# Kernel optimization log

Hardware: AMD Instinct MI355X
Metric: run time of the kernel (lower is better)

The kernel has to match this reference:

```python
import jax, jax.numpy as jnp
import numpy as np

B, N, C_IN, C_OUT, K = 16, 4096, 3, 64, 20
EPS = 1e-5


def setup_inputs() -> dict:
    key = jax.random.key(0)
    ks = jax.random.split(key, 6)
    x = jax.random.normal(ks[0], (B * N, C_IN), dtype=jnp.float32)
    batch = jnp.repeat(jnp.arange(B, dtype=jnp.int32), N)
    # MLP([2*C_IN, C_OUT, C_OUT]) per PyG: Linear -> BatchNorm -> ReLU -> Linear (plain last)
    w1 = jax.random.normal(ks[1], (2 * C_IN, C_OUT), dtype=jnp.float32) / np.sqrt(2 * C_IN)
    b1 = jnp.zeros((C_OUT,), dtype=jnp.float32)
    gamma = jnp.ones((C_OUT,), dtype=jnp.float32)
    beta = jnp.zeros((C_OUT,), dtype=jnp.float32)
    w2 = jax.random.normal(ks[2], (C_OUT, C_OUT), dtype=jnp.float32) / np.sqrt(C_OUT)
    b2 = jnp.zeros((C_OUT,), dtype=jnp.float32)
    return {"x": x, "batch": batch, "w1": w1, "b1": b1,
            "gamma": gamma, "beta": beta, "w2": w2, "b2": b2}


def reference(x, batch, w1, b1, gamma, beta, w2, b2):
    # batch is sorted with equal-size clouds -> reshape to [B, N, C]
    xb = x.reshape(B, N, C_IN)
    # pairwise squared distances within each cloud: [B, N, N]
    sq = jnp.sum(xb * xb, axis=-1)
    d = sq[:, :, None] + sq[:, None, :] - 2.0 * jnp.einsum('bnc,bmc->bnm', xb, xb)
    # k nearest neighbors (self included, matching PyG knn): [B, N, K]
    idx = jax.lax.top_k(-d, K)[1]
    # gather neighbor features: [B, N, K, C]
    xj = jax.vmap(lambda pts, ind: pts[ind])(xb, idx)
    xi = xb[:, :, None, :]
    # edge features [x_i, x_j - x_i]: [B, N, K, 2C]
    e = jnp.concatenate([jnp.broadcast_to(xi, (B, N, K, C_IN)), xj - xi], axis=-1)
    # MLP: Linear -> BatchNorm(train mode) -> ReLU -> Linear
    h = e @ w1 + b1  # [B, N, K, C_OUT]
    mean = jnp.mean(h, axis=(0, 1, 2))
    var = jnp.var(h, axis=(0, 1, 2))
    h = (h - mean) * jax.lax.rsqrt(var + EPS) * gamma + beta
    h = jax.nn.relu(h)
    h = h @ w2 + b2
    # max aggregation over neighbors -> [B*N, C_OUT]
    return jnp.max(h, axis=2).reshape(B * N, C_OUT)
```

## Files before the change

### kernel.cpp

```cpp
#include <hip/hip_runtime.h>
#include <math.h>
#include <float.h>

#define B_   16
#define N_   4096
#define CIN  3
#define COUT 64
#define KNN  20
#define EPS_ 1e-5


__device__ __forceinline__ unsigned expand10(unsigned v) {
    v = (v | (v << 16)) & 0x030000FFu;
    v = (v | (v << 8))  & 0x0300F00Fu;
    v = (v | (v << 4))  & 0x030C30C3u;
    v = (v | (v << 2))  & 0x09249249u;
    return v;
}
__device__ __forceinline__ unsigned quant10(float v) {
    int q = (int)((v + 4.0f) * 128.0f);
    return (unsigned)min(1023, max(0, q));
}

__global__ __launch_bounds__(1024) void morton_bucket_kernel(
    const float* __restrict__ x, int* __restrict__ perm)
{
    __shared__ int hist[1024];
    __shared__ int scanbuf[1024];
    __shared__ int offs[1024];
    const int b = blockIdx.x, tid = threadIdx.x;
    const float* xb = x + (size_t)b * N_ * CIN;

    hist[tid] = 0;
    __syncthreads();

    int keys[4];
#pragma unroll
    for (int i = 0; i < 4; ++i) {
        int p = tid + i * 1024;
        float v0 = xb[p * 3 + 0], v1 = xb[p * 3 + 1], v2 = xb[p * 3 + 2];
        unsigned m = (expand10(quant10(v0)) << 2) |
                     (expand10(quant10(v1)) << 1) |
                      expand10(quant10(v2));
        keys[i] = (int)(m >> 20);
        atomicAdd(&hist[keys[i]], 1);
    }
    __syncthreads();

    int v = hist[tid];
    scanbuf[tid] = v;
    __syncthreads();
    for (int off = 1; off < 1024; off <<= 1) {
        int t = (tid >= off) ? scanbuf[tid - off] : 0;
        __syncthreads();
        scanbuf[tid] += t;
        __syncthreads();
    }
    offs[tid] = scanbuf[tid] - v;
    __syncthreads();

#pragma unroll
    for (int i = 0; i < 4; ++i) {
        int p = tid + i * 1024;
        int pos = atomicAdd(&offs[keys[i]], 1);
        perm[b * N_ + pos] = p;
    }
}

__global__ __launch_bounds__(512) void knn_f64_kernel(
    const float* __restrict__ x, const int* __restrict__ perm,
    int* __restrict__ idx_out, double* __restrict__ stats)
{
    extern __shared__ __align__(16) char smem[];
    float4* pts = (float4*)smem;
    unsigned short* j16 = (unsigned short*)(smem + 65536);
    double* scr = (double*)smem;

    const int b    = blockIdx.y;
    const int tid  = threadIdx.x;
    const int wave = tid >> 6;
    const int lane = tid & 63;
    const int r    = wave >> 2;
    const int q    = wave & 3;
    const float* xb = x + (size_t)b * N_ * CIN;

    for (int p = tid; p < N_; p += 512) {
        int j = perm[b * N_ + p];
        float v0 = xb[j * 3 + 0], v1 = xb[j * 3 + 1], v2 = xb[j * 3 + 2];
        float sq = __fadd_rn(__fadd_rn(__fmul_rn(v0, v0),
                                       __fmul_rn(v1, v1)),
                             __fmul_rn(v2, v2));
        pts[p] = make_float4(v0, v1, v2, sq);
        j16[p] = (unsigned short)j;
    }
    __syncthreads();

    const int rowg = blockIdx.x * 128 + r * 64;
    const float4 xf = pts[rowg + lane];
    const int jrow  = j16[rowg + lane];
    const float sqi = xf.w;

    auto mkd = [&](float4 p) -> float {
        float dot = __fadd_rn(__fadd_rn(__fmul_rn(xf.x, p.x),
                                        __fmul_rn(xf.y, p.y)),
                              __fmul_rn(xf.z, p.z));
        return __fsub_rn(__fadd_rn(sqi, p.w), __fmul_rn(2.0f, dot));
    };
    auto sortable = [&](float d) -> unsigned {
        unsigned u = __float_as_uint(d);
        return u ^ (0x80000000u | (unsigned)((int)u >> 31));
    };

    double bk[KNN];
#pragma unroll
    for (int k = 0; k < KNN; ++k) bk[k] = 1e300;

    auto insert = [&](double key) {
        if (key < bk[KNN - 1]) {
            double m = key;
#pragma unroll
            for (int k = 0; k < KNN; ++k) {
                double old = bk[k];
                bk[k] = fmin(m, old);
                m     = fmax(old, m);
            }
        }
    };

    const int ta = rowg >> 2;
#pragma unroll
    for (int k = 0; k < KNN; ++k) {
        int p = 4 * ((ta + k) & 1023) + q;
        float4 a = pts[p];
        insert(fma((double)sortable(mkd(a)), 4096.0,
                   (double)(unsigned)j16[p]));
    }

    float d19f;
    {
        unsigned s19 = (unsigned)trunc(bk[KNN - 1] * (1.0 / 4096.0));
        unsigned u = (s19 >= 0x80000000u) ? (s19 ^ 0x80000000u) : ~s19;
        d19f = __uint_as_float(u);
    }

    for (int s = 0; s < 1024; s += 4) {
        int v0 = ((s + 0) * 509) & 1023;
        int v1 = ((s + 1) * 509) & 1023;
        int v2 = ((s + 2) * 509) & 1023;
        int v3 = ((s + 3) * 509) & 1023;
        int p0 = 4 * ((ta + v0) & 1023) + q;
        int p1 = 4 * ((ta + v1) & 1023) + q;
        int p2 = 4 * ((ta + v2) & 1023) + q;
        int p3 = 4 * ((ta + v3) & 1023) + q;
        float4 a0 = pts[p0];
        float4 a1 = pts[p1];
        float4 a2 = pts[p2];
        float4 a3 = pts[p3];
        float d0 = mkd(a0), d1 = mkd(a1), d2 = mkd(a2), d3 = mkd(a3);
        d0 = (v0 < 20) ? INFINITY : d0;
        d1 = (v1 < 20) ? INFINITY : d1;
        d2 = (v2 < 20) ? INFINITY : d2;
        d3 = (v3 < 20) ? INFINITY : d3;
        if ((d0 <= d19f) | (d1 <= d19f) | (d2 <= d19f) | (d3 <= d19f)) {
            unsigned j0 = j16[p0], j1 = j16[p1], j2 = j16[p2], j3 = j16[p3];
            insert(fma((double)sortable(d0), 4096.0, (double)j0));
            insert(fma((double)sortable(d1), 4096.0, (double)j1));
            insert(fma((double)sortable(d2), 4096.0, (double)j2));
            insert(fma((double)sortable(d3), 4096.0, (double)j3));
            unsigned s19 = (unsigned)trunc(bk[KNN - 1] * (1.0 / 4096.0));
            unsigned u = (s19 >= 0x80000000u) ? (s19 ^ 0x80000000u) : ~s19;
            d19f = __uint_as_float(u);
        }
    }
    __syncthreads();

    if (q & 1) {
        int base = ((r * 2 + (q >> 1)) * 64 + lane) * KNN;
#pragma unroll
        for (int k = 0; k < KNN; ++k) scr[base + k] = bk[k];
    }
    __syncthreads();
    if (!(q & 1)) {
        int base = ((r * 2 + (q >> 1)) * 64 + lane) * KNN;
#pragma unroll
        for (int k = 0; k < KNN; ++k) insert(scr[base + k]);
    }
    __syncthreads();
    if (q == 2) {
        int base = ((r * 2 + 1) * 64 + lane) * KNN;
#pragma unroll
        for (int k = 0; k < KNN; ++k) scr[base + k] = bk[k];
    }
    __syncthreads();
    if (q == 0) {
        int base = ((r * 2 + 1) * 64 + lane) * KNN;
#pragma unroll
        for (int k = 0; k < KNN; ++k) insert(scr[base + k]);

        const long long row = (long long)b * N_ + jrow;
        int bi[KNN];
#pragma unroll
        for (int k = 0; k < KNN; ++k) {
            double sp = trunc(bk[k] * (1.0 / 4096.0));
            bi[k] = (int)(bk[k] - sp * 4096.0);
        }
#pragma unroll
        for (int k = 0; k < KNN; ++k) idx_out[row * KNN + k] = bi[k];

        float acc[27];
#pragma unroll
        for (int t = 0; t < 27; ++t) acc[t] = 0.0f;
#pragma unroll
        for (int k = 0; k < KNN; ++k) {
            const float* pj = xb + bi[k] * 3;
            float e[6] = { xf.x, xf.y, xf.z,
                           pj[0] - xf.x, pj[1] - xf.y, pj[2] - xf.z };
            int t = 6;
#pragma unroll
            for (int a = 0; a < 6; ++a) {
                acc[a] += e[a];
#pragma unroll
                for (int bb = a; bb < 6; ++bb) acc[t++] += e[a] * e[bb];
            }
        }
#pragma unroll
        for (int t = 0; t < 27; ++t) {
            float v = acc[t];
            v += __shfl_down(v, 32); v += __shfl_down(v, 16);
            v += __shfl_down(v, 8);  v += __shfl_down(v, 4);
            v += __shfl_down(v, 2);  v += __shfl_down(v, 1);
            acc[t] = v;
        }
        if (lane == 0) {
#pragma unroll
            for (int t = 0; t < 27; ++t) atomicAdd(&stats[t], (double)acc[t]);
        }
    }
}

__global__ void bn_prep_kernel(
    const double* __restrict__ stats,
    const float* __restrict__ w1, const float* __restrict__ b1,
    const float* __restrict__ gamma, const float* __restrict__ beta,
    float* __restrict__ scale_shift)
{
    const int c = threadIdx.x;
    double s[6], S[6][6];
#pragma unroll
    for (int a = 0; a < 6; ++a) s[a] = stats[a];
    int t = 6;
#pragma unroll
    for (int a = 0; a < 6; ++a)
#pragma unroll
        for (int bb = a; bb < 6; ++bb) { S[a][bb] = stats[t]; S[bb][a] = stats[t]; ++t; }

    const double M = (double)B_ * N_ * KNN;
    double wc[6];
#pragma unroll
    for (int j = 0; j < 6; ++j) wc[j] = (double)w1[j * COUT + c];
    const double b1c = (double)b1[c];

    double sw = 0.0;
#pragma unroll
    for (int j = 0; j < 6; ++j) sw += s[j] * wc[j];
    double mean = sw / M + b1c;

    double qq = 0.0;
#pragma unroll
    for (int a = 0; a < 6; ++a)
#pragma unroll
        for (int bb = 0; bb < 6; ++bb) qq += S[a][bb] * wc[a] * wc[bb];
    double ex2 = (qq + 2.0 * b1c * sw) / M + b1c * b1c;
    double var = ex2 - mean * mean;

    double sc = (double)gamma[c] / sqrt(var + (double)EPS_);
    double sh = (double)beta[c] - mean * sc;
    scale_shift[c]        = (float)sc;
    scale_shift[COUT + c] = (float)sh;
}

typedef __attribute__((ext_vector_type(8))) short short8;
typedef __attribute__((ext_vector_type(4))) float f32x4;

__device__ __forceinline__ unsigned short f2bf_rn(float f) {
    unsigned u = __float_as_uint(f);
    unsigned lsb = (u >> 16) & 1u;
    return (unsigned short)((u + 0x7FFFu + lsb) >> 16);
}
__device__ __forceinline__ float bf2f(unsigned short h) {
    return __uint_as_float(((unsigned)h) << 16);
}

__global__ __launch_bounds__(256) void mlp_max_kernel(
    const float* __restrict__ x, const int* __restrict__ idx,
    const float* __restrict__ w1, const float* __restrict__ b1,
    const float* __restrict__ scale_shift,
    const float* __restrict__ w2, const float* __restrict__ b2,
    float* __restrict__ out)
{
    __shared__ __align__(16) unsigned short hbuf[4][2][16][136];
    __shared__ int idxs[4][320];

    const int tid  = threadIdx.x;
    const int wv   = tid >> 6;
    const int lane = tid & 63;
    const int g    = lane >> 4;
    const int r15  = lane & 15;

    const int R     = (blockIdx.x * 4 + wv) * 16;
    const int bbase = (R >> 12) << 12;

    {
        const int* ip = idx + (size_t)R * KNN;
#pragma unroll
        for (int i = 0; i < 5; ++i)
            idxs[wv][lane + i * 64] = ip[lane + i * 64];
    }

    const int c  = lane;
    const float sc = scale_shift[c];
    const float sh = scale_shift[COUT + c];
    float w1p[6];
#pragma unroll
    for (int j = 0; j < 6; ++j) w1p[j] = w1[j * COUT + c] * sc;
    const float b1p = fmaf(b1[c], sc, sh);
    const float dw0 = w1p[0] - w1p[3];
    const float dw1 = w1p[1] - w1p[4];
    const float dw2 = w1p[2] - w1p[5];

    short8 Wh[2][4], Wl[2][4];
#pragma unroll
    for (int t = 0; t < 2; ++t)
#pragma unroll
        for (int n = 0; n < 4; ++n) {
            short8 hv, lv;
#pragma unroll
            for (int jj = 0; jj < 8; ++jj) {
                float w = w2[(t * 32 + g * 8 + jj) * COUT + n * 16 + r15];
                unsigned short hi = f2bf_rn(w);
                unsigned short lo = f2bf_rn(w - bf2f(hi));
                hv[jj] = (short)hi;
                lv[jj] = (short)lo;
            }
            Wh[t][n] = hv;
            Wl[t][n] = lv;
        }

    float base[16];
#pragma unroll
    for (int r = 0; r < 16; ++r) {
        const float* pi = x + (size_t)(R + r) * 3;
        float v = b1p;
        v = fmaf(pi[0], dw0, v);
        v = fmaf(pi[1], dw1, v);
        v = fmaf(pi[2], dw2, v);
        base[r] = v;
    }

    float px[16], py[16], pz[16];
#pragma unroll
    for (int r = 0; r < 16; ++r) {
        int j = idxs[wv][r * KNN];
        const float* pj = x + (size_t)(bbase + j) * 3;
        px[r] = pj[0]; py[r] = pj[1]; pz[r] = pj[2];
    }

    f32x4 mx[4];
#pragma unroll
    for (int n = 0; n < 4; ++n) {
        mx[n][0] = -INFINITY; mx[n][1] = -INFINITY;
        mx[n][2] = -INFINITY; mx[n][3] = -INFINITY;
    }

    for (int k = 0; k < KNN; ++k) {
        unsigned short* hb = &hbuf[wv][k & 1][0][0];

#pragma unroll
        for (int r = 0; r < 16; ++r) {
            float h = base[r];
            h = fmaf(px[r], w1p[3], h);
            h = fmaf(py[r], w1p[4], h);
            h = fmaf(pz[r], w1p[5], h);
            h = fmaxf(h, 0.0f);
            unsigned hu = __float_as_uint(h);
            unsigned short hi = (unsigned short)(hu >> 16);
            float rem = h - __uint_as_float(hu & 0xFFFF0000u);
            unsigned short lo = (unsigned short)(__float_as_uint(rem) >> 16);
            hb[r * 136 + c]      = hi;
            hb[r * 136 + 64 + c] = lo;
        }

        if (k + 1 < KNN) {
#pragma unroll
            for (int r = 0; r < 16; ++r) {
                int j = idxs[wv][r * KNN + k + 1];
                const float* pj = x + (size_t)(bbase + j) * 3;
                px[r] = pj[0]; py[r] = pj[1]; pz[r] = pj[2];
            }
        }

        const unsigned short* rpnt = hb + r15 * 136;
        short8 Ah0 = *(const short8*)(rpnt + g * 8);
        short8 Ah1 = *(const short8*)(rpnt + 32 + g * 8);
        short8 Al0 = *(const short8*)(rpnt + 64 + g * 8);
        short8 Al1 = *(const short8*)(rpnt + 96 + g * 8);

#pragma unroll
        for (int n = 0; n < 4; ++n) {
            f32x4 a = {0.0f, 0.0f, 0.0f, 0.0f};
            a = __builtin_amdgcn_mfma_f32_16x16x32_bf16(Ah0, Wh[0][n], a, 0, 0, 0);
            a = __builtin_amdgcn_mfma_f32_16x16x32_bf16(Ah1, Wh[1][n], a, 0, 0, 0);
            a = __builtin_amdgcn_mfma_f32_16x16x32_bf16(Al0, Wh[0][n], a, 0, 0, 0);
            a = __builtin_amdgcn_mfma_f32_16x16x32_bf16(Al1, Wh[1][n], a, 0, 0, 0);
            a = __builtin_amdgcn_mfma_f32_16x16x32_bf16(Ah0, Wl[0][n], a, 0, 0, 0);
            a = __builtin_amdgcn_mfma_f32_16x16x32_bf16(Ah1, Wl[1][n], a, 0, 0, 0);
            mx[n][0] = fmaxf(mx[n][0], a[0]);
            mx[n][1] = fmaxf(mx[n][1], a[1]);
            mx[n][2] = fmaxf(mx[n][2], a[2]);
            mx[n][3] = fmaxf(mx[n][3], a[3]);
        }
    }

    float b2v[4];
#pragma unroll
    for (int n = 0; n < 4; ++n) b2v[n] = b2[n * 16 + r15];
#pragma unroll
    for (int n = 0; n < 4; ++n)
#pragma unroll
        for (int rr = 0; rr < 4; ++rr)
            out[(size_t)(R + g * 4 + rr) * COUT + n * 16 + r15] =
                mx[n][rr] + b2v[n];
}

extern "C" void kernel_launch(void* const* d_in, const int* in_sizes, int n_in,
                              void* d_out, int out_size, void* d_ws, size_t ws_size,
                              hipStream_t stream)
{
    const float* x     = (const float*)d_in[0];
    const float* w1    = (const float*)d_in[2];
    const float* b1    = (const float*)d_in[3];
    const float* gamma = (const float*)d_in[4];
    const float* beta  = (const float*)d_in[5];
    const float* w2    = (const float*)d_in[6];
    const float* b2    = (const float*)d_in[7];
    float* out = (float*)d_out;

    char*   ws          = (char*)d_ws;
    double* stats       = (double*)ws;
    float*  scale_shift = (float*)(ws + 256);
    int*    idx         = (int*)(ws + 1024);
    int*    perm        = (int*)(ws + 1024 + (size_t)B_ * N_ * KNN * 4);

    static int _lds_once = []() {
        (void)hipFuncSetAttribute((const void*)knn_f64_kernel,
                                  hipFuncAttributeMaxDynamicSharedMemorySize,
                                  131072);
        return 0;
    }();
    (void)_lds_once;

    hipMemsetAsync(stats, 0, 27 * sizeof(double), stream);
    morton_bucket_kernel<<<B_, 1024, 0, stream>>>(x, perm);
    knn_f64_kernel<<<dim3(32, 16), 512, 73728, stream>>>(x, perm, idx, stats);
    bn_prep_kernel<<<1, COUT, 0, stream>>>(stats, w1, b1, gamma, beta, scale_shift);
    mlp_max_kernel<<<(B_ * N_) / 64, 256, 0, stream>>>(x, idx, w1, b1, scale_shift,
                                                       w2, b2, out);
}
```

Before: 440.3 us.

## Gather neighbor coordinates cooperatively into LDS and fold stats memset into morton kernel

In the MLP kernel, each lane now loads one neighbor point per group of 4 neighbors into a double-buffered LDS staging area. Previously every lane issued redundant broadcast global loads for all 16 rows at each neighbor step. The bf16 hidden buffer becomes single-buffered, and the MFMA block is wrapped in s_setprio to favor matrix issue. The hipMemsetAsync of the BN stats is removed, and the zeroing moves into the morton bucket kernel to save one launch. The cost is extra LDS traffic and the reliance on in-wave LDS ordering without barriers.

```diff
diff --git a/kernel.cpp b/kernel.cpp
--- a/kernel.cpp
+++ b/kernel.cpp
@@ -23,13 +23,16 @@
 }
 
 __global__ __launch_bounds__(1024) void morton_bucket_kernel(
-    const float* __restrict__ x, int* __restrict__ perm)
+    const float* __restrict__ x, int* __restrict__ perm,
+    double* __restrict__ stats)
 {
     __shared__ int hist[1024];
     __shared__ int scanbuf[1024];
     __shared__ int offs[1024];
     const int b = blockIdx.x, tid = threadIdx.x;
     const float* xb = x + (size_t)b * N_ * CIN;
+
+    if (b == 0 && tid < 27) stats[tid] = 0.0;
 
     hist[tid] = 0;
     __syncthreads();
@@ -298,8 +301,9 @@
     const float* __restrict__ w2, const float* __restrict__ b2,
     float* __restrict__ out)
 {
-    __shared__ __align__(16) unsigned short hbuf[4][2][16][136];
+    __shared__ __align__(16) unsigned short hbuf[4][16][136];
     __shared__ int idxs[4][320];
+    __shared__ __align__(16) float4 sbuf[4][2][4][16];
 
     const int tid  = threadIdx.x;
     const int wv   = tid >> 6;
@@ -357,13 +361,17 @@
         base[r] = v;
     }
 
-    float px[16], py[16], pz[16];
-#pragma unroll
-    for (int r = 0; r < 16; ++r) {
-        int j = idxs[wv][r * KNN];
+    const int gr = lane >> 2;
+    const int gk = lane & 3;
+    auto gather_group = [&](int grp) {
+        int kk = grp * 4 + gk;
+        int j = idxs[wv][gr * KNN + kk];
         const float* pj = x + (size_t)(bbase + j) * 3;
-        px[r] = pj[0]; py[r] = pj[1]; pz[r] = pj[2];
-    }
+        sbuf[wv][grp & 1][gk][gr] =
+            make_float4(pj[0], pj[1], pj[2], 0.0f);
+    };
+
+    gather_group(0);
 
     f32x4 mx[4];
 #pragma unroll
@@ -372,52 +380,51 @@
         mx[n][2] = -INFINITY; mx[n][3] = -INFINITY;
     }
 
-    for (int k = 0; k < KNN; ++k) {
-        unsigned short* hb = &hbuf[wv][k & 1][0][0];
-
-#pragma unroll
-        for (int r = 0; r < 16; ++r) {
-            float h = base[r];
-            h = fmaf(px[r], w1p[3], h);
-            h = fmaf(py[r], w1p[4], h);
-            h = fmaf(pz[r], w1p[5], h);
-            h = fmaxf(h, 0.0f);
-            unsigned hu = __float_as_uint(h);
-            unsigned short hi = (unsigned short)(hu >> 16);
-            float rem = h - __uint_as_float(hu & 0xFFFF0000u);
-            unsigned short lo = (unsigned short)(__float_as_uint(rem) >> 16);
-            hb[r * 136 + c]      = hi;
-            hb[r * 136 + 64 + c] = lo;
-        }
-
-        if (k + 1 < KNN) {
+    unsigned short* hb = &hbuf[wv][0][0];
+    const unsigned short* rpnt = hb + r15 * 136;
+
+    for (int grp = 0; grp < 5; ++grp) {
+        if (grp + 1 < 5) gather_group(grp + 1);
+
+#pragma unroll
+        for (int kl = 0; kl < 4; ++kl) {
 #pragma unroll
             for (int r = 0; r < 16; ++r) {
-                int j = idxs[wv][r * KNN + k + 1];
-                const float* pj = x + (size_t)(bbase + j) * 3;
-                px[r] = pj[0]; py[r] = pj[1]; pz[r] = pj[2];
+                float4 pv = sbuf[wv][grp & 1][kl][r];
+                float h = base[r];
+                h = fmaf(pv.x, w1p[3], h);
+                h = fmaf(pv.y, w1p[4], h);
+                h = fmaf(pv.z, w1p[5], h);
+                h = fmaxf(h, 0.0f);
+                unsigned hu = __float_as_uint(h);
+                unsigned short hi = (unsigned short)(hu >> 16);
+                float rem = h - __uint_as_float(hu & 0xFFFF0000u);
+                unsigned short lo = (unsigned short)(__float_as_uint(rem) >> 16);
+                hb[r * 136 + c]      = hi;
+                hb[r * 136 + 64 + c] = lo;
             }
-        }
-
-        const unsigned short* rpnt = hb + r15 * 136;
-        short8 Ah0 = *(const short8*)(rpnt + g * 8);
-        short8 Ah1 = *(const short8*)(rpnt + 32 + g * 8);
-        short8 Al0 = *(const short8*)(rpnt + 64 + g * 8);
-        short8 Al1 = *(const short8*)(rpnt + 96 + g * 8);
-
-#pragma unroll
-        for (int n = 0; n < 4; ++n) {
-            f32x4 a = {0.0f, 0.0f, 0.0f, 0.0f};
-            a = __builtin_amdgcn_mfma_f32_16x16x32_bf16(Ah0, Wh[0][n], a, 0, 0, 0);
-            a = __builtin_amdgcn_mfma_f32_16x16x32_bf16(Ah1, Wh[1][n], a, 0, 0, 0);
-            a = __builtin_amdgcn_mfma_f32_16x16x32_bf16(Al0, Wh[0][n], a, 0, 0, 0);
-            a = __builtin_amdgcn_mfma_f32_16x16x32_bf16(Al1, Wh[1][n], a, 0, 0, 0);
-            a = __builtin_amdgcn_mfma_f32_16x16x32_bf16(Ah0, Wl[0][n], a, 0, 0, 0);
-            a = __builtin_amdgcn_mfma_f32_16x16x32_bf16(Ah1, Wl[1][n], a, 0, 0, 0);
-            mx[n][0] = fmaxf(mx[n][0], a[0]);
-            mx[n][1] = fmaxf(mx[n][1], a[1]);
-            mx[n][2] = fmaxf(mx[n][2], a[2]);
-            mx[n][3] = fmaxf(mx[n][3], a[3]);
+
+            short8 Ah0 = *(const short8*)(rpnt + g * 8);
+            short8 Ah1 = *(const short8*)(rpnt + 32 + g * 8);
+            short8 Al0 = *(const short8*)(rpnt + 64 + g * 8);
+            short8 Al1 = *(const short8*)(rpnt + 96 + g * 8);
+
+            __builtin_amdgcn_s_setprio(1);
+#pragma unroll
+            for (int n = 0; n < 4; ++n) {
+                f32x4 a = {0.0f, 0.0f, 0.0f, 0.0f};
+                a = __builtin_amdgcn_mfma_f32_16x16x32_bf16(Ah0, Wh[0][n], a, 0, 0, 0);
+                a = __builtin_amdgcn_mfma_f32_16x16x32_bf16(Ah1, Wh[1][n], a, 0, 0, 0);
+                a = __builtin_amdgcn_mfma_f32_16x16x32_bf16(Al0, Wh[0][n], a, 0, 0, 0);
+                a = __builtin_amdgcn_mfma_f32_16x16x32_bf16(Al1, Wh[1][n], a, 0, 0, 0);
+                a = __builtin_amdgcn_mfma_f32_16x16x32_bf16(Ah0, Wl[0][n], a, 0, 0, 0);
+                a = __builtin_amdgcn_mfma_f32_16x16x32_bf16(Ah1, Wl[1][n], a, 0, 0, 0);
+                mx[n][0] = fmaxf(mx[n][0], a[0]);
+                mx[n][1] = fmaxf(mx[n][1], a[1]);
+                mx[n][2] = fmaxf(mx[n][2], a[2]);
+                mx[n][3] = fmaxf(mx[n][3], a[3]);
+            }
+            __builtin_amdgcn_s_setprio(0);
         }
     }
 
@@ -459,8 +466,7 @@
     }();
     (void)_lds_once;
 
-    hipMemsetAsync(stats, 0, 27 * sizeof(double), stream);
-    morton_bucket_kernel<<<B_, 1024, 0, stream>>>(x, perm);
+    morton_bucket_kernel<<<B_, 1024, 0, stream>>>(x, perm, stats);
     knn_f64_kernel<<<dim3(32, 16), 512, 73728, stream>>>(x, perm, idx, stats);
     bn_prep_kernel<<<1, COUT, 0, stream>>>(stats, w1, b1, gamma, beta, scale_shift);
     mlp_max_kernel<<<(B_ * N_) / 64, 256, 0, stream>>>(x, idx, w1, b1, scale_shift,
```

Result: no change. 437.7 us (-0.6%).
